# Kernel tuning notes

Measured on AMD Instinct MI355X. Metric: run time of the kernel, lower is better.

## Reference

```python
import jax, jax.numpy as jnp
import numpy as np

N = 12288
IN_F = 128
OUT_F = 64
ALPHA = 0.2  # LeakyReLU negative slope
NEG_INF = -9e15


def setup_inputs() -> dict:
    key = jax.random.key(0)
    k1, k2, k3, k4 = jax.random.split(key, 4)
    input = jax.random.normal(k1, (N, IN_F), dtype=jnp.float32)
    adj = jax.random.randint(k2, (N, N), 0, 2, dtype=jnp.int32)
    # xavier-uniform-ish init with gain 1.414
    limW = 1.414 * np.sqrt(6.0 / (IN_F + OUT_F))
    W = jax.random.uniform(k3, (IN_F, OUT_F), dtype=jnp.float32, minval=-limW, maxval=limW)
    lima = 1.414 * np.sqrt(6.0 / (2 * OUT_F + 1))
    a = jax.random.uniform(k4, (2 * OUT_F, 1), dtype=jnp.float32, minval=-lima, maxval=lima)
    return {"input": input, "adj": adj, "W": W, "a": a}


def reference(input, adj, W, a):
    # h: (N, out_features)
    h = input @ W
    # broadcast attention logits: e[i,j] = leakyrelu(h_i . a1 + h_j . a2)
    Wh1 = h @ a[:OUT_F, :]          # (N, 1)
    Wh2 = h @ a[OUT_F:, :]          # (N, 1)
    e = Wh1 + Wh2.T                  # (N, N)
    e = jnp.where(e > 0, e, ALPHA * e)  # leaky relu
    # mask by adjacency, row softmax
    attention = jnp.where(adj > 0, e, NEG_INF)
    attention = jax.nn.softmax(attention, axis=1)
    # dropout is identity in eval mode (training=False)
    h_prime = attention @ h          # (N, out_features)
    return jax.nn.elu(h_prime)
```

## Files before the change

### kernel.cpp

```cpp
#include <hip/hip_runtime.h>

#define NN 12288
#define OUTF 64
#define ALPHA 0.2f
#define C1 6.0f
#define KSP 8
#define KRANGE (NN / KSP)
#define ITERS (KRANGE / 64)

typedef unsigned short u16;
typedef unsigned int u32;
typedef unsigned long long u64;
typedef _Float16 half8 __attribute__((ext_vector_type(8)));
typedef float floatx4 __attribute__((ext_vector_type(4)));
typedef int intx4 __attribute__((ext_vector_type(4)));

union H16 { u16 u; _Float16 h; };
__device__ __forceinline__ u16 f2h(float f) { H16 c; c.h = (_Float16)f; return c.u; }

__device__ __forceinline__ void g2l16(const void* g, void* l) {
  __builtin_amdgcn_global_load_lds(
      (const __attribute__((address_space(1))) void*)g,
      (__attribute__((address_space(3))) void*)l, 16, 0, 0);
}

__global__ __launch_bounds__(256) void k1_prep(
    const float* __restrict__ inp, const float* __restrict__ W, const float* __restrict__ a,
    u16* __restrict__ e1h, u16* __restrict__ thh,
    float* __restrict__ f1g, float* __restrict__ f2g, u16* __restrict__ Btf)
{
  __shared__ float Wl[128 * 64];
  __shared__ float hsm[64][65];
  __shared__ float e1sm[64], e2sm[64];
  const int tid = threadIdx.x, wave = tid >> 6, lane = tid & 63;
  const int b = blockIdx.x;
  for (int t = tid; t < 2048; t += 256)
    ((float4*)Wl)[t] = ((const float4*)W)[t];
  const float a1l = a[lane], a2l = a[OUTF + lane];
  __syncthreads();
  for (int jl = 0; jl < 16; ++jl) {
    const int jn = wave * 16 + jl;
    const int j = b * 64 + jn;
    const float4* xp = (const float4*)(inp + (size_t)j * 128);
    float h = 0.f;
#pragma unroll
    for (int c4 = 0; c4 < 32; ++c4) {
      float4 v = xp[c4];
      const int k = c4 * 4;
      h += v.x * Wl[k * 64 + lane] + v.y * Wl[(k + 1) * 64 + lane]
         + v.z * Wl[(k + 2) * 64 + lane] + v.w * Wl[(k + 3) * 64 + lane];
    }
    float p1 = h * a1l, p2 = h * a2l;
#pragma unroll
    for (int off = 32; off > 0; off >>= 1) { p1 += __shfl_xor(p1, off); p2 += __shfl_xor(p2, off); }
    hsm[jn][lane] = h;
    if (lane == 0) {
      const float s1 = p1, s2 = p2;
      const float e1 = expf(s2 - C1), e2 = expf(ALPHA * s2);
      e1sm[jn] = e1; e2sm[jn] = e2;
      e1h[j] = f2h(e1);
      thh[j] = f2h(expf(-s1 - C1));
      f1g[j] = expf(s1 + C1);
      f2g[j] = expf(ALPHA * s1);
    }
  }
  __syncthreads();
  for (int cc = tid; cc < 1280; cc += 256) {
    const int s = cc / 640, rem = cc - s * 640;
    const int n = rem >> 6, l = rem & 63;
    const int r = n * 16 + (l & 15);
    const int jb = s * 32 + (l >> 4) * 8;
    u32 wpk[4];
#pragma unroll
    for (int p = 0; p < 4; ++p) {
      u16 hh[2];
#pragma unroll
      for (int q2 = 0; q2 < 2; ++q2) {
        const int jj = jb + p * 2 + q2;
        float v;
        if (r < 64)        v = e1sm[jj] * hsm[jj][r];
        else if (r == 64)  v = e1sm[jj];
        else if (r < 80)   v = 0.f;
        else if (r < 144)  v = e2sm[jj] * hsm[jj][r - 80];
        else if (r == 144) v = e2sm[jj];
        else               v = 0.f;
        hh[q2] = f2h(v);
      }
      wpk[p] = (u32)hh[0] | ((u32)hh[1] << 16);
    }
    ((uint4*)Btf)[(size_t)((b * 2 + s) * 10 + n) * 64 + l] = make_uint4(wpk[0], wpk[1], wpk[2], wpk[3]);
  }
}

#define PACK_MASKS(dst1, dst2, AJ, EVV)                                                    \
  {                                                                                        \
    u32 ev8[8] = {EVV.x & 0xFFFFu, EVV.x >> 16, EVV.y & 0xFFFFu, EVV.y >> 16,              \
                  EVV.z & 0xFFFFu, EVV.z >> 16, EVV.w & 0xFFFFu, EVV.w >> 16};             \
    _Pragma("unroll")                                                                      \
    for (int p = 0; p < 4; ++p) {                                                          \
      const int av[8] = {AJ[p][0].x, AJ[p][0].y, AJ[p][0].z, AJ[p][0].w,                   \
                         AJ[p][1].x, AJ[p][1].y, AJ[p][1].z, AJ[p][1].w};                  \
      u32 b1 = 0, b2 = 0;                                                                  \
      _Pragma("unroll")                                                                    \
      for (int e = 0; e < 8; ++e) {                                                        \
        const bool nbr = av[e] > 0;                                                        \
        const bool up = ev8[e] > (u32)thu[p];                                              \
        b1 |= (u32)(nbr && up) << e;                                                       \
        b2 |= (u32)(nbr && !up) << e;                                                      \
      }                                                                                    \
      ((unsigned char*)&dst1[p * 32 + prow])[pcol] = (unsigned char)b1;                    \
      ((unsigned char*)&dst2[p * 32 + prow])[pcol] = (unsigned char)b2;                    \
    }                                                                                      \
  }

#define LOAD_ADJ(AJ, EV, koff)                                                             \
  {                                                                                        \
    _Pragma("unroll")                                                                      \
    for (int p = 0; p < 4; ++p) {                                                          \
      AJ[p][0] = __builtin_nontemporal_load((const intx4*)(aB + (size_t)p * 32 * NN + (koff)));      \
      AJ[p][1] = __builtin_nontemporal_load((const intx4*)(aB + (size_t)p * 32 * NN + (koff) + 4));  \
    }                                                                                      \
    EV = *(const uint4*)(eB + (koff));                                                     \
  }

#define DMA_B(buf, slab)                                                                   \
  {                                                                                        \
    const char* src = (const char*)(Btf + ((size_t)(k0 >> 5) + (slab) * 2) * 5120);        \
    _Pragma("unroll")                                                                      \
    for (int i = 0; i < 5; ++i)                                                            \
      g2l16(src + i * 4096 + tid * 16, (char*)&sB[buf][0] + i * 4096 + wave * 1024);       \
  }

#define MFMA_BODY(CUR)                                                                     \
  {                                                                                        \
    u64 w1[2], w2[2];                                                                      \
    w1[0] = m1s[CUR][wave * 32 + lr];      w1[1] = m1s[CUR][wave * 32 + 16 + lr];          \
    w2[0] = m2s[CUR][wave * 32 + lr];      w2[1] = m2s[CUR][wave * 32 + 16 + lr];          \
    _Pragma("unroll")                                                                      \
    for (int h = 0; h < 2; ++h) {                                                          \
      const u32 sh = (u32)(h * 32 + quad * 8);                                             \
      union { half8 v; u16 s[8]; } A1[2], A2[2];                                           \
      const u32 m1a = (u32)(w1[0] >> sh) & 0xFFu, m2a = (u32)(w2[0] >> sh) & 0xFFu;        \
      const u32 m1b = (u32)(w1[1] >> sh) & 0xFFu, m2b = (u32)(w2[1] >> sh) & 0xFFu;        \
      _Pragma("unroll")                                                                    \
      for (int e = 0; e < 8; ++e) {                                                        \
        A1[0].s[e] = ((m1a >> e) & 1u) ? (u16)0x3C00 : (u16)0;                             \
        A2[0].s[e] = ((m2a >> e) & 1u) ? (u16)0x3C00 : (u16)0;                             \
        A1[1].s[e] = ((m1b >> e) & 1u) ? (u16)0x3C00 : (u16)0;                             \
        A2[1].s[e] = ((m2b >> e) & 1u) ? (u16)0x3C00 : (u16)0;                             \
      }                                                                                    \
      const u16* bp = &sB[CUR][h * 5120];                                                  \
      _Pragma("unroll")                                                                    \
      for (int n = 0; n < 10; ++n) {                                                       \
        half8 Bv = *(const half8*)(bp + (n * 64 + lane) * 8);                              \
        acc[0][n] = __builtin_amdgcn_mfma_f32_16x16x32_f16(n < 5 ? A1[0].v : A2[0].v, Bv,  \
                                                           acc[0][n], 0, 0, 0);            \
        acc[1][n] = __builtin_amdgcn_mfma_f32_16x16x32_f16(n < 5 ? A1[1].v : A2[1].v, Bv,  \
                                                           acc[1][n], 0, 0, 0);            \
      }                                                                                    \
    }                                                                                      \
  }

__global__ __launch_bounds__(256, 2) void k2_main(
    const int* __restrict__ adj, const u16* __restrict__ e1h, const u16* __restrict__ thh,
    const u16* __restrict__ Btf, float* __restrict__ part)
{
  __shared__ u16 sB[2][10240];
  __shared__ u64 m1s[2][128];
  __shared__ u64 m2s[2][128];
  const int tid = threadIdx.x;
  const int wave = tid >> 6, lane = tid & 63;
  const int quad = lane >> 4, lr = lane & 15;
  const int mpos = (int)blockIdx.x >> 3;
  const int ks = (int)blockIdx.x & 7;
  const int mbase = mpos * 128;
  const int k0 = ks * KRANGE;

  const int prow = tid >> 3, pcol = tid & 7;
  u16 thu[4];
#pragma unroll
  for (int p = 0; p < 4; ++p) thu[p] = thh[mbase + p * 32 + prow];
  const int* aB = adj + (size_t)(mbase + prow) * NN + k0 + pcol * 8;
  const u16* eB = e1h + k0 + pcol * 8;

  floatx4 acc[2][10];
#pragma unroll
  for (int t = 0; t < 2; ++t)
#pragma unroll
    for (int n = 0; n < 10; ++n) acc[t][n] = (floatx4){0.f, 0.f, 0.f, 0.f};

  intx4 ajb0[4][2], ajb1[4][2];
  uint4 ev0, ev1;

  DMA_B(0, 0)
  LOAD_ADJ(ajb0, ev0, 0)
  PACK_MASKS(m1s[0], m2s[0], ajb0, ev0)
  LOAD_ADJ(ajb1, ev1, 64)

  for (int it = 0; it < ITERS; it += 2) {
    __syncthreads();
    if (it + 1 < ITERS) {
      DMA_B(1, it + 1)
      PACK_MASKS(m1s[1], m2s[1], ajb1, ev1)
    }
    if (it + 2 < ITERS) LOAD_ADJ(ajb0, ev0, (it + 2) * 64)
    MFMA_BODY(0)
    __syncthreads();
    if (it + 2 < ITERS) {
      DMA_B(0, it + 2)
      PACK_MASKS(m1s[0], m2s[0], ajb0, ev0)
    }
    if (it + 3 < ITERS) LOAD_ADJ(ajb1, ev1, (it + 3) * 64)
    MFMA_BODY(1)
  }

  const int ks96 = ks * 96 + mpos;
#pragma unroll
  for (int t = 0; t < 2; ++t) {
    float* pp = part + ((size_t)ks96 * 128 + wave * 32 + t * 16 + quad * 4) * 132;
#pragma unroll
    for (int r = 0; r < 4; ++r) {
#pragma unroll
      for (int n = 0; n < 4; ++n)
        pp[r * 132 + n * 16 + lr] = acc[t][n][r];
#pragma unroll
      for (int n = 5; n < 9; ++n)
        pp[r * 132 + 64 + (n - 5) * 16 + lr] = acc[t][n][r];
      if (lr == 0) {
        pp[r * 132 + 128] = acc[t][4][r];
        pp[r * 132 + 129] = acc[t][9][r];
      }
    }
  }
}

__global__ __launch_bounds__(256) void k3_final(
    const float* __restrict__ part, const float* __restrict__ f1g,
    const float* __restrict__ f2g, float* __restrict__ out)
{
  const int gid = blockIdx.x * 256 + threadIdx.x;
  const int row = gid >> 6, col = gid & 63;
  const int mpos = row >> 7, r = row & 127;
  float n1 = 0.f, n2 = 0.f, d1 = 0.f, d2 = 0.f;
#pragma unroll
  for (int ks = 0; ks < KSP; ++ks) {
    const float* p = part + ((size_t)(ks * 96 + mpos) * 128 + r) * 132;
    n1 += p[col]; n2 += p[64 + col]; d1 += p[128]; d2 += p[129];
  }
  const float f1 = f1g[row], f2 = f2g[row];
  const float num = f1 * n1 + f2 * n2;
  const float den = fmaxf(f1 * d1 + f2 * d2, 1e-30f);
  const float x = num / den;
  out[gid] = x > 0.f ? x : (expf(x) - 1.f);
}

extern "C" void kernel_launch(void* const* d_in, const int* in_sizes, int n_in,
                              void* d_out, int out_size, void* d_ws, size_t ws_size,
                              hipStream_t stream) {
  const float* inp = (const float*)d_in[0];
  const int* adj = (const int*)d_in[1];
  const float* W = (const float*)d_in[2];
  const float* a = (const float*)d_in[3];

  char* ws = (char*)d_ws;
  u16* Btf = (u16*)ws;
  float* part = (float*)(ws + 3932160);
  char* tail = ws + 3932160 + 51904512;
  u16* e1h = (u16*)tail;
  u16* thh = e1h + NN;
  float* f1g = (float*)(thh + NN);
  float* f2g = f1g + NN;

  k1_prep<<<192, 256, 0, stream>>>(inp, W, a, e1h, thh, f1g, f2g, Btf);
  k2_main<<<768, 256, 0, stream>>>(adj, e1h, thh, Btf, part);
  k3_final<<<NN * OUTF / 256, 256, 0, stream>>>(part, f1g, f2g, (float*)d_out);
}
```

Baseline: 867.2 us.

## Process two k-slabs per barrier and pass adjacency masks via wave shuffles

Each wave now loads and packs the adjacency rows it consumes itself. The packed mask bits stay in registers and are redistributed with __shfl instead of going through LDS mask arrays. The main loop handles pairs of 64-wide slabs per stage with a four-slot B buffer in LDS, which halves the number of __syncthreads and doubles the DMA batch. The cost is more LDS (occupancy risk at two blocks per CU), more live registers for raw adjacency, and shuffle overhead in the compute stage.

```diff
diff --git a/kernel.cpp b/kernel.cpp
--- a/kernel.cpp
+++ b/kernel.cpp
@@ -6,7 +6,7 @@
 #define C1 6.0f
 #define KSP 8
 #define KRANGE (NN / KSP)
-#define ITERS (KRANGE / 64)
+#define PAIRS 12
 
 typedef unsigned short u16;
 typedef unsigned int u32;
@@ -92,71 +92,85 @@
   }
 }
 
-#define PACK_MASKS(dst1, dst2, AJ, EVV)                                                    \
-  {                                                                                        \
-    u32 ev8[8] = {EVV.x & 0xFFFFu, EVV.x >> 16, EVV.y & 0xFFFFu, EVV.y >> 16,              \
-                  EVV.z & 0xFFFFu, EVV.z >> 16, EVV.w & 0xFFFFu, EVV.w >> 16};             \
-    _Pragma("unroll")                                                                      \
-    for (int p = 0; p < 4; ++p) {                                                          \
-      const int av[8] = {AJ[p][0].x, AJ[p][0].y, AJ[p][0].z, AJ[p][0].w,                   \
-                         AJ[p][1].x, AJ[p][1].y, AJ[p][1].z, AJ[p][1].w};                  \
-      u32 b1 = 0, b2 = 0;                                                                  \
+
+#define LOAD_PAIR(pairIdx)                                                                 \
+  {                                                                                        \
+    _Pragma("unroll")                                                                      \
+    for (int s = 0; s < 2; ++s) {                                                          \
+      const int koff = (pairIdx) * 128 + s * 64;                                           \
       _Pragma("unroll")                                                                    \
-      for (int e = 0; e < 8; ++e) {                                                        \
-        const bool nbr = av[e] > 0;                                                        \
-        const bool up = ev8[e] > (u32)thu[p];                                              \
-        b1 |= (u32)(nbr && up) << e;                                                       \
-        b2 |= (u32)(nbr && !up) << e;                                                      \
+      for (int p = 0; p < 4; ++p) {                                                        \
+        raw[s][p][0] = __builtin_nontemporal_load((const intx4*)(aB + (size_t)p * 8 * NN + koff));     \
+        raw[s][p][1] = __builtin_nontemporal_load((const intx4*)(aB + (size_t)p * 8 * NN + koff + 4)); \
       }                                                                                    \
-      ((unsigned char*)&dst1[p * 32 + prow])[pcol] = (unsigned char)b1;                    \
-      ((unsigned char*)&dst2[p * 32 + prow])[pcol] = (unsigned char)b2;                    \
+      evr[s] = *(const uint4*)(eB + koff);                                                 \
     }                                                                                      \
   }
 
-#define LOAD_ADJ(AJ, EV, koff)                                                             \
-  {                                                                                        \
-    _Pragma("unroll")                                                                      \
-    for (int p = 0; p < 4; ++p) {                                                          \
-      AJ[p][0] = __builtin_nontemporal_load((const intx4*)(aB + (size_t)p * 32 * NN + (koff)));      \
-      AJ[p][1] = __builtin_nontemporal_load((const intx4*)(aB + (size_t)p * 32 * NN + (koff) + 4));  \
+#define PACK_PAIR(PK1, PK2)                                                                \
+  {                                                                                        \
+    _Pragma("unroll")                                                                      \
+    for (int s = 0; s < 2; ++s) {                                                          \
+      u32 ev8[8] = {evr[s].x & 0xFFFFu, evr[s].x >> 16, evr[s].y & 0xFFFFu, evr[s].y >> 16,\
+                    evr[s].z & 0xFFFFu, evr[s].z >> 16, evr[s].w & 0xFFFFu, evr[s].w >> 16};\
+      u32 o1 = 0, o2 = 0;                                                                  \
+      _Pragma("unroll")                                                                    \
+      for (int p = 0; p < 4; ++p) {                                                        \
+        const int av[8] = {raw[s][p][0].x, raw[s][p][0].y, raw[s][p][0].z, raw[s][p][0].w, \
+                           raw[s][p][1].x, raw[s][p][1].y, raw[s][p][1].z, raw[s][p][1].w};\
+        u32 b1 = 0, b2 = 0;                                                                \
+        _Pragma("unroll")                                                                  \
+        for (int e = 0; e < 8; ++e) {                                                      \
+          const bool nbr = av[e] > 0;                                                      \
+          const bool up = ev8[e] > (u32)thu[p];                                            \
+          b1 |= (u32)(nbr && up) << e;                                                     \
+          b2 |= (u32)(nbr && !up) << e;                                                    \
+        }                                                                                  \
+        o1 |= b1 << (8 * p);                                                               \
+        o2 |= b2 << (8 * p);                                                               \
+      }                                                                                    \
+      PK1[s] = o1; PK2[s] = o2;                                                            \
     }                                                                                      \
-    EV = *(const uint4*)(eB + (koff));                                                     \
-  }
-
-#define DMA_B(buf, slab)                                                                   \
-  {                                                                                        \
-    const char* src = (const char*)(Btf + ((size_t)(k0 >> 5) + (slab) * 2) * 5120);        \
-    _Pragma("unroll")                                                                      \
-    for (int i = 0; i < 5; ++i)                                                            \
-      g2l16(src + i * 4096 + tid * 16, (char*)&sB[buf][0] + i * 4096 + wave * 1024);       \
-  }
-
-#define MFMA_BODY(CUR)                                                                     \
-  {                                                                                        \
-    u64 w1[2], w2[2];                                                                      \
-    w1[0] = m1s[CUR][wave * 32 + lr];      w1[1] = m1s[CUR][wave * 32 + 16 + lr];          \
-    w2[0] = m2s[CUR][wave * 32 + lr];      w2[1] = m2s[CUR][wave * 32 + 16 + lr];          \
-    _Pragma("unroll")                                                                      \
-    for (int h = 0; h < 2; ++h) {                                                          \
-      const u32 sh = (u32)(h * 32 + quad * 8);                                             \
-      union { half8 v; u16 s[8]; } A1[2], A2[2];                                           \
-      const u32 m1a = (u32)(w1[0] >> sh) & 0xFFu, m2a = (u32)(w2[0] >> sh) & 0xFFu;        \
-      const u32 m1b = (u32)(w1[1] >> sh) & 0xFFu, m2b = (u32)(w2[1] >> sh) & 0xFFu;        \
+  }
+
+#define DMA_PAIR(pb, pairIdx)                                                              \
+  {                                                                                        \
+    const char* src = (const char*)(Btf + ((size_t)(k0 >> 5) + (size_t)(pairIdx) * 4) * 5120); \
+    _Pragma("unroll")                                                                      \
+    for (int i = 0; i < 10; ++i)                                                           \
+      g2l16(src + i * 4096 + tid * 16, (char*)&sB[(pb) * 2][0] + i * 4096 + wave * 1024);  \
+  }
+
+#define COMPUTE_PAIR(pb, PK1, PK2)                                                         \
+  {                                                                                        \
+    _Pragma("unroll")                                                                      \
+    for (int s = 0; s < 2; ++s) {                                                          \
       _Pragma("unroll")                                                                    \
-      for (int e = 0; e < 8; ++e) {                                                        \
-        A1[0].s[e] = ((m1a >> e) & 1u) ? (u16)0x3C00 : (u16)0;                             \
-        A2[0].s[e] = ((m2a >> e) & 1u) ? (u16)0x3C00 : (u16)0;                             \
-        A1[1].s[e] = ((m1b >> e) & 1u) ? (u16)0x3C00 : (u16)0;                             \
-        A2[1].s[e] = ((m2b >> e) & 1u) ? (u16)0x3C00 : (u16)0;                             \
-      }                                                                                    \
-      const u16* bp = &sB[CUR][h * 5120];                                                  \
-      _Pragma("unroll")                                                                    \
-      for (int n = 0; n < 10; ++n) {                                                       \
-        half8 Bv = *(const half8*)(bp + (n * 64 + lane) * 8);                              \
-        acc[0][n] = __builtin_amdgcn_mfma_f32_16x16x32_f16(n < 5 ? A1[0].v : A2[0].v, Bv,  \
-                                                           acc[0][n], 0, 0, 0);            \
-        acc[1][n] = __builtin_amdgcn_mfma_f32_16x16x32_f16(n < 5 ? A1[1].v : A2[1].v, Bv,  \
-                                                           acc[1][n], 0, 0, 0);            \
+      for (int h = 0; h < 2; ++h) {                                                        \
+        const int sl = ((lr & 7) << 3) | (h * 4 + quad);                                   \
+        const u32 v1 = (u32)__shfl((int)PK1[s], sl);                                       \
+        const u32 v2 = (u32)__shfl((int)PK2[s], sl);                                       \
+        union { half8 v; u16 s[8]; } A1[2], A2[2];                                         \
+        _Pragma("unroll")                                                                  \
+        for (int t = 0; t < 2; ++t) {                                                      \
+          const u32 sh2 = 8u * (u32)(t * 2 + (lr >> 3));                                   \
+          const u32 m1 = (v1 >> sh2) & 0xFFu;                                              \
+          const u32 m2 = (v2 >> sh2) & 0xFFu;                                              \
+          _Pragma("unroll")                                                                \
+          for (int e = 0; e < 8; ++e) {                                                    \
+            A1[t].s[e] = ((m1 >> e) & 1u) ? (u16)0x3C00 : (u16)0;                          \
+            A2[t].s[e] = ((m2 >> e) & 1u) ? (u16)0x3C00 : (u16)0;                          \
+          }                                                                                \
+        }                                                                                  \
+        const u16* bp = &sB[(pb) * 2 + s][h * 5120];                                       \
+        _Pragma("unroll")                                                                  \
+        for (int n = 0; n < 10; ++n) {                                                     \
+          half8 Bv = *(const half8*)(bp + (n * 64 + lane) * 8);                            \
+          acc[0][n] = __builtin_amdgcn_mfma_f32_16x16x32_f16(n < 5 ? A1[0].v : A2[0].v, Bv,\
+                                                             acc[0][n], 0, 0, 0);          \
+          acc[1][n] = __builtin_amdgcn_mfma_f32_16x16x32_f16(n < 5 ? A1[1].v : A2[1].v, Bv,\
+                                                             acc[1][n], 0, 0, 0);          \
+        }                                                                                  \
       }                                                                                    \
     }                                                                                      \
   }
@@ -165,9 +179,7 @@
     const int* __restrict__ adj, const u16* __restrict__ e1h, const u16* __restrict__ thh,
     const u16* __restrict__ Btf, float* __restrict__ part)
 {
-  __shared__ u16 sB[2][10240];
-  __shared__ u64 m1s[2][128];
-  __shared__ u64 m2s[2][128];
+  __shared__ u16 sB[4][10240];
   const int tid = threadIdx.x;
   const int wave = tid >> 6, lane = tid & 63;
   const int quad = lane >> 4, lr = lane & 15;
@@ -176,11 +188,11 @@
   const int mbase = mpos * 128;
   const int k0 = ks * KRANGE;
 
-  const int prow = tid >> 3, pcol = tid & 7;
+  const int prow8 = lane >> 3, pcol = lane & 7;
   u16 thu[4];
 #pragma unroll
-  for (int p = 0; p < 4; ++p) thu[p] = thh[mbase + p * 32 + prow];
-  const int* aB = adj + (size_t)(mbase + prow) * NN + k0 + pcol * 8;
+  for (int p = 0; p < 4; ++p) thu[p] = thh[mbase + wave * 32 + p * 8 + prow8];
+  const int* aB = adj + (size_t)(mbase + wave * 32 + prow8) * NN + k0 + pcol * 8;
   const u16* eB = e1h + k0 + pcol * 8;
 
   floatx4 acc[2][10];
@@ -189,29 +201,30 @@
 #pragma unroll
     for (int n = 0; n < 10; ++n) acc[t][n] = (floatx4){0.f, 0.f, 0.f, 0.f};
 
-  intx4 ajb0[4][2], ajb1[4][2];
-  uint4 ev0, ev1;
-
-  DMA_B(0, 0)
-  LOAD_ADJ(ajb0, ev0, 0)
-  PACK_MASKS(m1s[0], m2s[0], ajb0, ev0)
-  LOAD_ADJ(ajb1, ev1, 64)
-
-  for (int it = 0; it < ITERS; it += 2) {
+  intx4 raw[2][4][2];
+  uint4 evr[2];
+  u32 pk1a[2], pk2a[2], pk1b[2], pk2b[2];
+
+  DMA_PAIR(0, 0)
+  LOAD_PAIR(0)
+  PACK_PAIR(pk1a, pk2a)
+  LOAD_PAIR(1)
+
+  for (int cp = 0; cp < PAIRS; cp += 2) {
     __syncthreads();
-    if (it + 1 < ITERS) {
-      DMA_B(1, it + 1)
-      PACK_MASKS(m1s[1], m2s[1], ajb1, ev1)
-    }
-    if (it + 2 < ITERS) LOAD_ADJ(ajb0, ev0, (it + 2) * 64)
-    MFMA_BODY(0)
+    if (cp + 1 < PAIRS) {
+      DMA_PAIR(1, cp + 1)
+      PACK_PAIR(pk1b, pk2b)
+    }
+    if (cp + 2 < PAIRS) LOAD_PAIR(cp + 2)
+    COMPUTE_PAIR(0, pk1a, pk2a)
     __syncthreads();
-    if (it + 2 < ITERS) {
-      DMA_B(0, it + 2)
-      PACK_MASKS(m1s[0], m2s[0], ajb0, ev0)
-    }
-    if (it + 3 < ITERS) LOAD_ADJ(ajb1, ev1, (it + 3) * 64)
-    MFMA_BODY(1)
+    if (cp + 2 < PAIRS) {
+      DMA_PAIR(0, cp + 2)
+      PACK_PAIR(pk1a, pk2a)
+    }
+    if (cp + 3 < PAIRS) LOAD_PAIR(cp + 3)
+    COMPUTE_PAIR(1, pk1b, pk2b)
   }
 
   const int ks96 = ks * 96 + mpos;
```

Measured after the change: 932.0 us. 1.07x slower.
